# Kernel tuning notes

Measured on AMD Instinct MI355X. Metric: run time of the kernel, lower is better.

Reference implementation:

```python
import jax, jax.numpy as jnp
import numpy as np

N, E = 50000, 800000
D_IN, D_H, D_E, D_P = 128, 64, 64, 64


def _glorot(key, shape):
    lim = (6.0 / (shape[0] + shape[1])) ** 0.5
    return jax.random.uniform(key, shape, jnp.float32, -lim, lim)


def setup_inputs() -> dict:
    key = jax.random.key(0)
    ks = jax.random.split(key, 8)
    x = jax.random.normal(ks[0], (N, D_IN), jnp.float32)
    edge_index = jax.random.randint(ks[1], (2, E), 0, N, dtype=jnp.int64)
    return {
        "x": x,
        "edge_index": edge_index,
        "W1": _glorot(ks[2], (D_IN, D_H)),
        "b1": jnp.zeros((D_H,), jnp.float32),
        "W2": _glorot(ks[3], (D_H, D_E)),
        "b2": jnp.zeros((D_E,), jnp.float32),
        "Wp1": _glorot(ks[4], (D_E, D_E)),
        "bp1": jnp.zeros((D_E,), jnp.float32),
        "Wp2": _glorot(ks[5], (D_E, D_P)),
        "bp2": jnp.zeros((D_P,), jnp.float32),
    }


def gcn_conv(x, src, dst, W, b):
    # PyG GCNConv: h = D^{-1/2}(A+I)D^{-1/2} (x W) + b, self-loops already in src/dst
    n = x.shape[0]
    h = x @ W  # transform first (out_dim < in_dim -> cheaper messages)
    deg = jax.ops.segment_sum(jnp.ones_like(dst, dtype=h.dtype), dst, num_segments=n)
    dinv = jnp.where(deg > 0, jax.lax.rsqrt(deg), 0.0)
    norm = dinv[src] * dinv[dst]  # [E']
    out = jax.ops.segment_sum(h[src] * norm[:, None], dst, num_segments=n)
    return out + b


def reference(x, edge_index, W1, b1, W2, b2, Wp1, bp1, Wp2, bp2):
    n = x.shape[0]
    loops = jnp.arange(n, dtype=edge_index.dtype)
    src = jnp.concatenate([edge_index[0], loops])
    dst = jnp.concatenate([edge_index[1], loops])
    h = jax.nn.relu(gcn_conv(x, src, dst, W1, b1))
    z = gcn_conv(h, src, dst, W2, b2)
    p = jax.nn.relu(z @ Wp1 + bp1) @ Wp2 + bp2
    return (z, p)
```

## Files before the change

kernel.cpp:

```cpp
#include <hip/hip_runtime.h>
#include <hip/hip_fp16.h>

#define DIN 128
#define DH 64
#define NBINS 512
#define BIN_SHIFT 7
#define BIN_NODES 128
#define ETILE 4096
#define EBUF 4096

__device__ inline unsigned pack_half2(float a, float b) {
  __half2 h = __floats2half2_rn(a, b);
  return *(unsigned*)&h;
}
__device__ inline float2 unpack_half2(unsigned u) {
  __half2 h = *(__half2*)&u;
  return __half22float2(h);
}

__global__ __launch_bounds__(512) void k_zero(int* __restrict__ p, int n) {
  int i = blockIdx.x * blockDim.x + threadIdx.x;
  if (i < n) p[i] = 0;
}

__global__ __launch_bounds__(256) void k_fusedA(const float* __restrict__ x,
                                                const float* __restrict__ W1,
                                                __half* __restrict__ g1,
                                                const int* __restrict__ dst,
                                                int* __restrict__ binTot,
                                                int n, int e, int gG) {
  __shared__ float xsT[32][132];
  __shared__ float ws[32 * 64];
  __shared__ int hh[NBINS];
  int t = threadIdx.x;
  int bid = blockIdx.x;

  if (bid >= gG) {
    int b = bid - gG;
    for (int i = t; i < NBINS; i += 256) hh[i] = 0;
    __syncthreads();
    int lo = b * ETILE, hi = lo + ETILE; if (hi > e) hi = e;
    for (int i = lo + t; i < hi; i += 256) atomicAdd(&hh[dst[i] >> BIN_SHIFT], 1);
    __syncthreads();
    for (int i = t; i < NBINS; i += 256) if (hh[i]) atomicAdd(&binTot[i], hh[i]);
    return;
  }

  int row0 = bid * 128;
  int rg = t >> 4, cg = t & 15;
  int r0 = rg * 8, c0 = cg * 4;
  int lr = t >> 3, kq = t & 7;
  float4 acc[8];
#pragma unroll
  for (int i = 0; i < 8; ++i) acc[i] = make_float4(0.f, 0.f, 0.f, 0.f);

  for (int kc = 0; kc < DIN; kc += 32) {
#pragma unroll
    for (int it = 0; it < 4; ++it) {
      int r = it * 32 + lr;
      int gr = row0 + r;
      float4 v = make_float4(0.f, 0.f, 0.f, 0.f);
      if (gr < n) v = *(const float4*)&x[(size_t)gr * DIN + kc + kq * 4];
      xsT[kq * 4 + 0][r] = v.x;
      xsT[kq * 4 + 1][r] = v.y;
      xsT[kq * 4 + 2][r] = v.z;
      xsT[kq * 4 + 3][r] = v.w;
    }
#pragma unroll
    for (int j = 0; j < 8; ++j) ws[t + j * 256] = W1[(size_t)kc * 64 + t + j * 256];
    __syncthreads();
#pragma unroll
    for (int k = 0; k < 32; ++k) {
      float4 xa = *(const float4*)&xsT[k][r0];
      float4 xb = *(const float4*)&xsT[k][r0 + 4];
      float4 wv = *(const float4*)&ws[k * 64 + c0];
      float xr[8] = {xa.x, xa.y, xa.z, xa.w, xb.x, xb.y, xb.z, xb.w};
#pragma unroll
      for (int i = 0; i < 8; ++i) {
        acc[i].x = fmaf(xr[i], wv.x, acc[i].x);
        acc[i].y = fmaf(xr[i], wv.y, acc[i].y);
        acc[i].z = fmaf(xr[i], wv.z, acc[i].z);
        acc[i].w = fmaf(xr[i], wv.w, acc[i].w);
      }
    }
    __syncthreads();
  }
#pragma unroll
  for (int i = 0; i < 8; ++i) {
    int gr = row0 + r0 + i;
    if (gr < n) {
      uint2 u;
      u.x = pack_half2(acc[i].x, acc[i].y);
      u.y = pack_half2(acc[i].z, acc[i].w);
      *(uint2*)&g1[(size_t)gr * 64 + c0] = u;
    }
  }
}

__global__ __launch_bounds__(512) void k_binscan(const int* __restrict__ binTot,
                                                 int* __restrict__ binOff,
                                                 int* __restrict__ binCur, int e) {
  __shared__ int sm[NBINS];
  int t = threadIdx.x;
  int v = binTot[t];
  sm[t] = v;
  __syncthreads();
  for (int ofs = 1; ofs < NBINS; ofs <<= 1) {
    int u = (t >= ofs) ? sm[t - ofs] : 0;
    __syncthreads();
    sm[t] += u;
    __syncthreads();
  }
  int ex = sm[t] - v;
  binOff[t] = ex;
  binCur[t] = ex;
  if (t == NBINS - 1) binOff[NBINS] = sm[NBINS - 1];
}

__global__ __launch_bounds__(256) void k_scatter2(const int* __restrict__ src,
                                                  const int* __restrict__ dst,
                                                  int* __restrict__ binCur,
                                                  int* __restrict__ sp, int e) {
  __shared__ int hh[NBINS];
  __shared__ int base[NBINS];
  int t = threadIdx.x;
  for (int i = t; i < NBINS; i += 256) hh[i] = 0;
  __syncthreads();
  int lo = blockIdx.x * ETILE, hi = lo + ETILE; if (hi > e) hi = e;
  for (int i = lo + t; i < hi; i += 256) atomicAdd(&hh[dst[i] >> BIN_SHIFT], 1);
  __syncthreads();
  for (int i = t; i < NBINS; i += 256) {
    int c = hh[i];
    base[i] = c ? atomicAdd(&binCur[i], c) : 0;
  }
  __syncthreads();
  for (int i = t; i < NBINS; i += 256) hh[i] = 0;
  __syncthreads();
  for (int i = lo + t; i < hi; i += 256) {
    int d = dst[i];
    int bn = d >> BIN_SHIFT;
    int pos = base[bn] + atomicAdd(&hh[bn], 1);
    sp[pos] = (src[i] << BIN_SHIFT) | (d & (BIN_NODES - 1));
  }
}

__global__ __launch_bounds__(256) void k_bincsr(const int* __restrict__ sp,
                                                const int* __restrict__ binOff,
                                                int* __restrict__ off,
                                                float* __restrict__ dinv,
                                                int* __restrict__ srcs,
                                                int n, int e) {
  __shared__ int dl[BIN_NODES];
  __shared__ int sc[BIN_NODES];
  __shared__ int curl[BIN_NODES];
  __shared__ int ebuf[EBUF];
  int b = blockIdx.x, t = threadIdx.x;
  if (t < BIN_NODES) dl[t] = 0;
  __syncthreads();
  int e0 = binOff[b];
  int e1 = binOff[b + 1];
  for (int i = e0 + t; i < e1; i += 256) {
    int u = sp[i];
    int k = i - e0;
    if (k < EBUF) ebuf[k] = u;
    atomicAdd(&dl[u & (BIN_NODES - 1)], 1);
  }
  __syncthreads();
  if (t < BIN_NODES) sc[t] = dl[t];
  __syncthreads();
  for (int ofs = 1; ofs < BIN_NODES; ofs <<= 1) {
    int v = (t < BIN_NODES && t >= ofs) ? sc[t - ofs] : 0;
    __syncthreads();
    if (t < BIN_NODES) sc[t] += v;
    __syncthreads();
  }
  int nbase = b * BIN_NODES;
  if (t < BIN_NODES) {
    int ex = e0 + sc[t] - dl[t];
    curl[t] = ex;
    int node = nbase + t;
    if (node < n) {
      off[node] = ex;
      dinv[node] = rsqrtf((float)(dl[t] + 1));
    }
  }
  if (b == 0 && t == 0) off[n] = e;
  __syncthreads();
  for (int i = e0 + t; i < e1; i += 256) {
    int k = i - e0;
    int u = (k < EBUF) ? ebuf[k] : sp[i];
    int l = u & (BIN_NODES - 1);
    int pos = atomicAdd(&curl[l], 1);
    srcs[pos] = u >> BIN_SHIFT;
  }
}

__global__ __launch_bounds__(256) void k_agg(const __half* __restrict__ gh,
                                             const int* __restrict__ off,
                                             const int* __restrict__ srcs,
                                             const float* __restrict__ dinv,
                                             const float* __restrict__ bias,
                                             __half* __restrict__ out, int n, int relu) {
  int gid = blockIdx.x * 4 + (threadIdx.x >> 6);
  if (gid >= n) return;
  gid = __builtin_amdgcn_readfirstlane(gid);
  int lane = threadIdx.x & 63;
  int grp = lane >> 4;
  int d4 = (lane & 15) * 4;
  float di = dinv[gid];
  float4 acc = make_float4(0.f, 0.f, 0.f, 0.f);
  if (grp == 0) {
    uint2 raw = *(const uint2*)(gh + (size_t)gid * DH + d4);
    float2 f0 = unpack_half2(raw.x), f1 = unpack_half2(raw.y);
    float s = di * di;
    acc.x = f0.x * s; acc.y = f0.y * s; acc.z = f1.x * s; acc.w = f1.y * s;
  }
  int b0 = off[gid], b1 = off[gid + 1];
  int j = b0 + grp;
  for (; j + 12 < b1; j += 16) {
    int s0 = srcs[j], s1 = srcs[j + 4], s2 = srcs[j + 8], s3 = srcs[j + 12];
    float w0 = dinv[s0] * di, w1 = dinv[s1] * di;
    float w2 = dinv[s2] * di, w3 = dinv[s3] * di;
    uint2 r0 = *(const uint2*)(gh + (size_t)s0 * DH + d4);
    uint2 r1 = *(const uint2*)(gh + (size_t)s1 * DH + d4);
    uint2 r2 = *(const uint2*)(gh + (size_t)s2 * DH + d4);
    uint2 r3 = *(const uint2*)(gh + (size_t)s3 * DH + d4);
    float2 a0 = unpack_half2(r0.x), a1 = unpack_half2(r0.y);
    float2 c0 = unpack_half2(r1.x), c1 = unpack_half2(r1.y);
    float2 e0 = unpack_half2(r2.x), e1 = unpack_half2(r2.y);
    float2 g0 = unpack_half2(r3.x), g1 = unpack_half2(r3.y);
    acc.x = fmaf(a0.x, w0, acc.x); acc.y = fmaf(a0.y, w0, acc.y);
    acc.z = fmaf(a1.x, w0, acc.z); acc.w = fmaf(a1.y, w0, acc.w);
    acc.x = fmaf(c0.x, w1, acc.x); acc.y = fmaf(c0.y, w1, acc.y);
    acc.z = fmaf(c1.x, w1, acc.z); acc.w = fmaf(c1.y, w1, acc.w);
    acc.x = fmaf(e0.x, w2, acc.x); acc.y = fmaf(e0.y, w2, acc.y);
    acc.z = fmaf(e1.x, w2, acc.z); acc.w = fmaf(e1.y, w2, acc.w);
    acc.x = fmaf(g0.x, w3, acc.x); acc.y = fmaf(g0.y, w3, acc.y);
    acc.z = fmaf(g1.x, w3, acc.z); acc.w = fmaf(g1.y, w3, acc.w);
  }
  for (; j + 4 < b1; j += 8) {
    int sa = srcs[j], sb = srcs[j + 4];
    float wa = dinv[sa] * di, wb = dinv[sb] * di;
    uint2 ra = *(const uint2*)(gh + (size_t)sa * DH + d4);
    uint2 rb = *(const uint2*)(gh + (size_t)sb * DH + d4);
    float2 a0 = unpack_half2(ra.x), a1 = unpack_half2(ra.y);
    float2 c0 = unpack_half2(rb.x), c1 = unpack_half2(rb.y);
    acc.x = fmaf(a0.x, wa, acc.x); acc.y = fmaf(a0.y, wa, acc.y);
    acc.z = fmaf(a1.x, wa, acc.z); acc.w = fmaf(a1.y, wa, acc.w);
    acc.x = fmaf(c0.x, wb, acc.x); acc.y = fmaf(c0.y, wb, acc.y);
    acc.z = fmaf(c1.x, wb, acc.z); acc.w = fmaf(c1.y, wb, acc.w);
  }
  if (j < b1) {
    int s = srcs[j];
    float w = dinv[s] * di;
    uint2 r = *(const uint2*)(gh + (size_t)s * DH + d4);
    float2 f0 = unpack_half2(r.x), f1 = unpack_half2(r.y);
    acc.x = fmaf(f0.x, w, acc.x); acc.y = fmaf(f0.y, w, acc.y);
    acc.z = fmaf(f1.x, w, acc.z); acc.w = fmaf(f1.y, w, acc.w);
  }
  acc.x += __shfl_xor(acc.x, 16, 64); acc.x += __shfl_xor(acc.x, 32, 64);
  acc.y += __shfl_xor(acc.y, 16, 64); acc.y += __shfl_xor(acc.y, 32, 64);
  acc.z += __shfl_xor(acc.z, 16, 64); acc.z += __shfl_xor(acc.z, 32, 64);
  acc.w += __shfl_xor(acc.w, 16, 64); acc.w += __shfl_xor(acc.w, 32, 64);
  if (lane < 16) {
    if (bias) {
      float4 bv = *(const float4*)&bias[d4];
      acc.x += bv.x; acc.y += bv.y; acc.z += bv.z; acc.w += bv.w;
    }
    if (relu) {
      acc.x = fmaxf(acc.x, 0.f); acc.y = fmaxf(acc.y, 0.f);
      acc.z = fmaxf(acc.z, 0.f); acc.w = fmaxf(acc.w, 0.f);
    }
    uint2 u;
    u.x = pack_half2(acc.x, acc.y);
    u.y = pack_half2(acc.z, acc.w);
    *(uint2*)&out[(size_t)gid * DH + d4] = u;
  }
}

template <bool RELU, bool INHALF>
__global__ __launch_bounds__(256) void k_gemm_rt(const void* __restrict__ Av,
                                                 const float* __restrict__ W,
                                                 const float* __restrict__ bias,
                                                 float* __restrict__ out, int n) {
  constexpr int KC = 32;
  constexpr int MP = 132;
  __shared__ float xsT[KC][MP];
  __shared__ float ws[KC * 64];
  __shared__ float bs[64];
  int t = threadIdx.x;
  if (t < 64) bs[t] = bias[t];
  int row0 = blockIdx.x * 128;
  int rg = t >> 4, cg = t & 15;
  int r0 = rg * 8, c0 = cg * 4;
  float4 acc[8];
#pragma unroll
  for (int i = 0; i < 8; ++i) acc[i] = make_float4(0.f, 0.f, 0.f, 0.f);

  int lr = t >> 3;
  int kq = t & 7;

  for (int kc = 0; kc < DH; kc += KC) {
#pragma unroll
    for (int it = 0; it < 4; ++it) {
      int r = it * 32 + lr;
      int gr = row0 + r;
      float4 v = make_float4(0.f, 0.f, 0.f, 0.f);
      if (gr < n) {
        if (INHALF) {
          uint2 u = *(const uint2*)((const __half*)Av + (size_t)gr * DH + kc + kq * 4);
          float2 f0 = unpack_half2(u.x), f1 = unpack_half2(u.y);
          v = make_float4(f0.x, f0.y, f1.x, f1.y);
        } else {
          v = *(const float4*)&((const float*)Av)[(size_t)gr * DH + kc + kq * 4];
        }
      }
      xsT[kq * 4 + 0][r] = v.x;
      xsT[kq * 4 + 1][r] = v.y;
      xsT[kq * 4 + 2][r] = v.z;
      xsT[kq * 4 + 3][r] = v.w;
    }
#pragma unroll
    for (int j = 0; j < 8; ++j) {
      int idx = t + j * 256;
      ws[idx] = W[(size_t)kc * 64 + idx];
    }
    __syncthreads();
#pragma unroll
    for (int k = 0; k < KC; ++k) {
      float4 xa = *(const float4*)&xsT[k][r0];
      float4 xb = *(const float4*)&xsT[k][r0 + 4];
      float4 wv = *(const float4*)&ws[k * 64 + c0];
      float xr[8] = {xa.x, xa.y, xa.z, xa.w, xb.x, xb.y, xb.z, xb.w};
#pragma unroll
      for (int i = 0; i < 8; ++i) {
        acc[i].x = fmaf(xr[i], wv.x, acc[i].x);
        acc[i].y = fmaf(xr[i], wv.y, acc[i].y);
        acc[i].z = fmaf(xr[i], wv.z, acc[i].z);
        acc[i].w = fmaf(xr[i], wv.w, acc[i].w);
      }
    }
    __syncthreads();
  }

  float4 bv = *(const float4*)&bs[c0];
#pragma unroll
  for (int i = 0; i < 8; ++i) {
    int gr = row0 + r0 + i;
    if (gr < n) {
      float4 o = acc[i];
      o.x += bv.x; o.y += bv.y; o.z += bv.z; o.w += bv.w;
      if (RELU) {
        o.x = fmaxf(o.x, 0.f); o.y = fmaxf(o.y, 0.f);
        o.z = fmaxf(o.z, 0.f); o.w = fmaxf(o.w, 0.f);
      }
      *(float4*)&out[(size_t)gr * DH + c0] = o;
    }
  }
}

extern "C" void kernel_launch(void* const* d_in, const int* in_sizes, int n_in,
                              void* d_out, int out_size, void* d_ws, size_t ws_size,
                              hipStream_t stream) {
  const float* x   = (const float*)d_in[0];
  const int*   ei  = (const int*)d_in[1];
  const float* W1  = (const float*)d_in[2];
  const float* b1  = (const float*)d_in[3];
  const float* W2  = (const float*)d_in[4];
  const float* b2  = (const float*)d_in[5];
  const float* Wp1 = (const float*)d_in[6];
  const float* bp1 = (const float*)d_in[7];
  const float* Wp2 = (const float*)d_in[8];
  const float* bp2 = (const float*)d_in[9];

  int n = in_sizes[0] / DIN;
  int e = in_sizes[1] / 2;
  const int* src = ei;
  const int* dst = ei + e;

  int nblkE = (e + ETILE - 1) / ETILE;
  int nbBins = (n + BIN_NODES - 1) / BIN_NODES;
  int gG = (n + 127) / 128;

  char* ws = (char*)d_ws;
  __half* gtab   = (__half*)ws;
  __half* htab   = (__half*)(ws + ((size_t)7 << 20));
  char*   ctrl   = ws + ((size_t)14 << 20);
  int*    binTot = (int*)(ctrl);
  int*    binOff = (int*)(ctrl + 4096);
  int*    binCur = (int*)(ctrl + 8192);
  int*    off    = (int*)(ctrl + 16384);
  float*  dinv   = (float*)(ctrl + 16384 + (1 << 18));
  int*    sp     = (int*)(ctrl + 16384 + (2 << 18));
  int*    srcs   = sp + e;
  float*  tbuf   = (float*)(ws + ((size_t)24 << 20));

  float* zout = (float*)d_out;
  float* pout = zout + (size_t)n * DH;

  k_zero<<<1, 512, 0, stream>>>(binTot, NBINS);

  k_fusedA<<<gG + nblkE, 256, 0, stream>>>(x, W1, gtab, dst, binTot, n, e, gG);

  k_binscan<<<1, 512, 0, stream>>>(binTot, binOff, binCur, e);

  k_scatter2<<<nblkE, 256, 0, stream>>>(src, dst, binCur, sp, e);

  k_bincsr<<<nbBins, 256, 0, stream>>>(sp, binOff, off, dinv, srcs, n, e);

  k_agg<<<(n + 3) / 4, 256, 0, stream>>>(gtab, off, srcs, dinv, b1, htab, n, 1);

  k_agg<<<(n + 3) / 4, 256, 0, stream>>>(htab, off, srcs, dinv, nullptr, gtab, n, 0);

  k_gemm_rt<false, true ><<<gG, 256, 0, stream>>>(gtab, W2, b2, zout, n);
  k_gemm_rt<true,  false><<<gG, 256, 0, stream>>>(zout, Wp1, bp1, tbuf, n);
  k_gemm_rt<false, false><<<gG, 256, 0, stream>>>(tbuf, Wp2, bp2, pout, n);
}
```

Measured before the change: 141.8 us.

## Prescale features by dinv to remove per-edge dinv gathers in aggregation

```diff
diff --git a/kernel.cpp b/kernel.cpp
--- a/kernel.cpp
+++ b/kernel.cpp
@@ -23,78 +23,16 @@
   if (i < n) p[i] = 0;
 }
 
-__global__ __launch_bounds__(256) void k_fusedA(const float* __restrict__ x,
-                                                const float* __restrict__ W1,
-                                                __half* __restrict__ g1,
-                                                const int* __restrict__ dst,
-                                                int* __restrict__ binTot,
-                                                int n, int e, int gG) {
-  __shared__ float xsT[32][132];
-  __shared__ float ws[32 * 64];
+__global__ __launch_bounds__(256) void k_hist(const int* __restrict__ dst,
+                                              int* __restrict__ binTot, int e) {
   __shared__ int hh[NBINS];
   int t = threadIdx.x;
-  int bid = blockIdx.x;
-
-  if (bid >= gG) {
-    int b = bid - gG;
-    for (int i = t; i < NBINS; i += 256) hh[i] = 0;
-    __syncthreads();
-    int lo = b * ETILE, hi = lo + ETILE; if (hi > e) hi = e;
-    for (int i = lo + t; i < hi; i += 256) atomicAdd(&hh[dst[i] >> BIN_SHIFT], 1);
-    __syncthreads();
-    for (int i = t; i < NBINS; i += 256) if (hh[i]) atomicAdd(&binTot[i], hh[i]);
-    return;
-  }
-
-  int row0 = bid * 128;
-  int rg = t >> 4, cg = t & 15;
-  int r0 = rg * 8, c0 = cg * 4;
-  int lr = t >> 3, kq = t & 7;
-  float4 acc[8];
-#pragma unroll
-  for (int i = 0; i < 8; ++i) acc[i] = make_float4(0.f, 0.f, 0.f, 0.f);
-
-  for (int kc = 0; kc < DIN; kc += 32) {
-#pragma unroll
-    for (int it = 0; it < 4; ++it) {
-      int r = it * 32 + lr;
-      int gr = row0 + r;
-      float4 v = make_float4(0.f, 0.f, 0.f, 0.f);
-      if (gr < n) v = *(const float4*)&x[(size_t)gr * DIN + kc + kq * 4];
-      xsT[kq * 4 + 0][r] = v.x;
-      xsT[kq * 4 + 1][r] = v.y;
-      xsT[kq * 4 + 2][r] = v.z;
-      xsT[kq * 4 + 3][r] = v.w;
-    }
-#pragma unroll
-    for (int j = 0; j < 8; ++j) ws[t + j * 256] = W1[(size_t)kc * 64 + t + j * 256];
-    __syncthreads();
-#pragma unroll
-    for (int k = 0; k < 32; ++k) {
-      float4 xa = *(const float4*)&xsT[k][r0];
-      float4 xb = *(const float4*)&xsT[k][r0 + 4];
-      float4 wv = *(const float4*)&ws[k * 64 + c0];
-      float xr[8] = {xa.x, xa.y, xa.z, xa.w, xb.x, xb.y, xb.z, xb.w};
-#pragma unroll
-      for (int i = 0; i < 8; ++i) {
-        acc[i].x = fmaf(xr[i], wv.x, acc[i].x);
-        acc[i].y = fmaf(xr[i], wv.y, acc[i].y);
-        acc[i].z = fmaf(xr[i], wv.z, acc[i].z);
-        acc[i].w = fmaf(xr[i], wv.w, acc[i].w);
-      }
-    }
-    __syncthreads();
-  }
-#pragma unroll
-  for (int i = 0; i < 8; ++i) {
-    int gr = row0 + r0 + i;
-    if (gr < n) {
-      uint2 u;
-      u.x = pack_half2(acc[i].x, acc[i].y);
-      u.y = pack_half2(acc[i].z, acc[i].w);
-      *(uint2*)&g1[(size_t)gr * 64 + c0] = u;
-    }
-  }
+  for (int i = t; i < NBINS; i += 256) hh[i] = 0;
+  __syncthreads();
+  int lo = blockIdx.x * ETILE, hi = lo + ETILE; if (hi > e) hi = e;
+  for (int i = lo + t; i < hi; i += 256) atomicAdd(&hh[dst[i] >> BIN_SHIFT], 1);
+  __syncthreads();
+  for (int i = t; i < NBINS; i += 256) if (hh[i]) atomicAdd(&binTot[i], hh[i]);
 }
 
 __global__ __launch_bounds__(512) void k_binscan(const int* __restrict__ binTot,
@@ -195,12 +133,72 @@
   }
 }
 
-__global__ __launch_bounds__(256) void k_agg(const __half* __restrict__ gh,
-                                             const int* __restrict__ off,
-                                             const int* __restrict__ srcs,
-                                             const float* __restrict__ dinv,
-                                             const float* __restrict__ bias,
-                                             __half* __restrict__ out, int n, int relu) {
+__global__ __launch_bounds__(256) void k_gemm1d(const float* __restrict__ x,
+                                                const float* __restrict__ W1,
+                                                const float* __restrict__ dinv,
+                                                __half* __restrict__ g1, int n) {
+  __shared__ float xsT[32][132];
+  __shared__ float ws[32 * 64];
+  int t = threadIdx.x;
+  int row0 = blockIdx.x * 128;
+  int rg = t >> 4, cg = t & 15;
+  int r0 = rg * 8, c0 = cg * 4;
+  int lr = t >> 3, kq = t & 7;
+  float4 acc[8];
+#pragma unroll
+  for (int i = 0; i < 8; ++i) acc[i] = make_float4(0.f, 0.f, 0.f, 0.f);
+
+  for (int kc = 0; kc < DIN; kc += 32) {
+#pragma unroll
+    for (int it = 0; it < 4; ++it) {
+      int r = it * 32 + lr;
+      int gr = row0 + r;
+      float4 v = make_float4(0.f, 0.f, 0.f, 0.f);
+      if (gr < n) v = *(const float4*)&x[(size_t)gr * DIN + kc + kq * 4];
+      xsT[kq * 4 + 0][r] = v.x;
+      xsT[kq * 4 + 1][r] = v.y;
+      xsT[kq * 4 + 2][r] = v.z;
+      xsT[kq * 4 + 3][r] = v.w;
+    }
+#pragma unroll
+    for (int j = 0; j < 8; ++j) ws[t + j * 256] = W1[(size_t)kc * 64 + t + j * 256];
+    __syncthreads();
+#pragma unroll
+    for (int k = 0; k < 32; ++k) {
+      float4 xa = *(const float4*)&xsT[k][r0];
+      float4 xb = *(const float4*)&xsT[k][r0 + 4];
+      float4 wv = *(const float4*)&ws[k * 64 + c0];
+      float xr[8] = {xa.x, xa.y, xa.z, xa.w, xb.x, xb.y, xb.z, xb.w};
+#pragma unroll
+      for (int i = 0; i < 8; ++i) {
+        acc[i].x = fmaf(xr[i], wv.x, acc[i].x);
+        acc[i].y = fmaf(xr[i], wv.y, acc[i].y);
+        acc[i].z = fmaf(xr[i], wv.z, acc[i].z);
+        acc[i].w = fmaf(xr[i], wv.w, acc[i].w);
+      }
+    }
+    __syncthreads();
+  }
+#pragma unroll
+  for (int i = 0; i < 8; ++i) {
+    int gr = row0 + r0 + i;
+    if (gr < n) {
+      float di = dinv[gr];
+      uint2 u;
+      u.x = pack_half2(acc[i].x * di, acc[i].y * di);
+      u.y = pack_half2(acc[i].z * di, acc[i].w * di);
+      *(uint2*)&g1[(size_t)gr * 64 + c0] = u;
+    }
+  }
+}
+
+__global__ __launch_bounds__(256) void k_agg2(const __half* __restrict__ gh,
+                                              const int* __restrict__ off,
+                                              const int* __restrict__ srcs,
+                                              const float* __restrict__ dinv,
+                                              const float* __restrict__ bias,
+                                              __half* __restrict__ out, int n,
+                                              int relu, int scaleout) {
   int gid = blockIdx.x * 4 + (threadIdx.x >> 6);
   if (gid >= n) return;
   gid = __builtin_amdgcn_readfirstlane(gid);
@@ -212,15 +210,12 @@
   if (grp == 0) {
     uint2 raw = *(const uint2*)(gh + (size_t)gid * DH + d4);
     float2 f0 = unpack_half2(raw.x), f1 = unpack_half2(raw.y);
-    float s = di * di;
-    acc.x = f0.x * s; acc.y = f0.y * s; acc.z = f1.x * s; acc.w = f1.y * s;
+    acc.x = f0.x; acc.y = f0.y; acc.z = f1.x; acc.w = f1.y;
   }
   int b0 = off[gid], b1 = off[gid + 1];
   int j = b0 + grp;
   for (; j + 12 < b1; j += 16) {
     int s0 = srcs[j], s1 = srcs[j + 4], s2 = srcs[j + 8], s3 = srcs[j + 12];
-    float w0 = dinv[s0] * di, w1 = dinv[s1] * di;
-    float w2 = dinv[s2] * di, w3 = dinv[s3] * di;
     uint2 r0 = *(const uint2*)(gh + (size_t)s0 * DH + d4);
     uint2 r1 = *(const uint2*)(gh + (size_t)s1 * DH + d4);
     uint2 r2 = *(const uint2*)(gh + (size_t)s2 * DH + d4);
@@ -229,40 +224,34 @@
     float2 c0 = unpack_half2(r1.x), c1 = unpack_half2(r1.y);
     float2 e0 = unpack_half2(r2.x), e1 = unpack_half2(r2.y);
     float2 g0 = unpack_half2(r3.x), g1 = unpack_half2(r3.y);
-    acc.x = fmaf(a0.x, w0, acc.x); acc.y = fmaf(a0.y, w0, acc.y);
-    acc.z = fmaf(a1.x, w0, acc.z); acc.w = fmaf(a1.y, w0, acc.w);
-    acc.x = fmaf(c0.x, w1, acc.x); acc.y = fmaf(c0.y, w1, acc.y);
-    acc.z = fmaf(c1.x, w1, acc.z); acc.w = fmaf(c1.y, w1, acc.w);
-    acc.x = fmaf(e0.x, w2, acc.x); acc.y = fmaf(e0.y, w2, acc.y);
-    acc.z = fmaf(e1.x, w2, acc.z); acc.w = fmaf(e1.y, w2, acc.w);
-    acc.x = fmaf(g0.x, w3, acc.x); acc.y = fmaf(g0.y, w3, acc.y);
-    acc.z = fmaf(g1.x, w3, acc.z); acc.w = fmaf(g1.y, w3, acc.w);
+    acc.x += a0.x + c0.x + e0.x + g0.x;
+    acc.y += a0.y + c0.y + e0.y + g0.y;
+    acc.z += a1.x + c1.x + e1.x + g1.x;
+    acc.w += a1.y + c1.y + e1.y + g1.y;
   }
   for (; j + 4 < b1; j += 8) {
     int sa = srcs[j], sb = srcs[j + 4];
-    float wa = dinv[sa] * di, wb = dinv[sb] * di;
     uint2 ra = *(const uint2*)(gh + (size_t)sa * DH + d4);
     uint2 rb = *(const uint2*)(gh + (size_t)sb * DH + d4);
     float2 a0 = unpack_half2(ra.x), a1 = unpack_half2(ra.y);
     float2 c0 = unpack_half2(rb.x), c1 = unpack_half2(rb.y);
-    acc.x = fmaf(a0.x, wa, acc.x); acc.y = fmaf(a0.y, wa, acc.y);
-    acc.z = fmaf(a1.x, wa, acc.z); acc.w = fmaf(a1.y, wa, acc.w);
-    acc.x = fmaf(c0.x, wb, acc.x); acc.y = fmaf(c0.y, wb, acc.y);
-    acc.z = fmaf(c1.x, wb, acc.z); acc.w = fmaf(c1.y, wb, acc.w);
+    acc.x += a0.x + c0.x;
+    acc.y += a0.y + c0.y;
+    acc.z += a1.x + c1.x;
+    acc.w += a1.y + c1.y;
   }
   if (j < b1) {
     int s = srcs[j];
-    float w = dinv[s] * di;
     uint2 r = *(const uint2*)(gh + (size_t)s * DH + d4);
     float2 f0 = unpack_half2(r.x), f1 = unpack_half2(r.y);
-    acc.x = fmaf(f0.x, w, acc.x); acc.y = fmaf(f0.y, w, acc.y);
-    acc.z = fmaf(f1.x, w, acc.z); acc.w = fmaf(f1.y, w, acc.w);
+    acc.x += f0.x; acc.y += f0.y; acc.z += f1.x; acc.w += f1.y;
   }
   acc.x += __shfl_xor(acc.x, 16, 64); acc.x += __shfl_xor(acc.x, 32, 64);
   acc.y += __shfl_xor(acc.y, 16, 64); acc.y += __shfl_xor(acc.y, 32, 64);
   acc.z += __shfl_xor(acc.z, 16, 64); acc.z += __shfl_xor(acc.z, 32, 64);
   acc.w += __shfl_xor(acc.w, 16, 64); acc.w += __shfl_xor(acc.w, 32, 64);
   if (lane < 16) {
+    acc.x *= di; acc.y *= di; acc.z *= di; acc.w *= di;
     if (bias) {
       float4 bv = *(const float4*)&bias[d4];
       acc.x += bv.x; acc.y += bv.y; acc.z += bv.z; acc.w += bv.w;
@@ -270,6 +259,9 @@
     if (relu) {
       acc.x = fmaxf(acc.x, 0.f); acc.y = fmaxf(acc.y, 0.f);
       acc.z = fmaxf(acc.z, 0.f); acc.w = fmaxf(acc.w, 0.f);
+    }
+    if (scaleout) {
+      acc.x *= di; acc.y *= di; acc.z *= di; acc.w *= di;
     }
     uint2 u;
     u.x = pack_half2(acc.x, acc.y);
@@ -399,18 +391,16 @@
   float* pout = zout + (size_t)n * DH;
 
   k_zero<<<1, 512, 0, stream>>>(binTot, NBINS);
-
-  k_fusedA<<<gG + nblkE, 256, 0, stream>>>(x, W1, gtab, dst, binTot, n, e, gG);
-
+  k_hist<<<nblkE, 256, 0, stream>>>(dst, binTot, e);
   k_binscan<<<1, 512, 0, stream>>>(binTot, binOff, binCur, e);
-
   k_scatter2<<<nblkE, 256, 0, stream>>>(src, dst, binCur, sp, e);
-
   k_bincsr<<<nbBins, 256, 0, stream>>>(sp, binOff, off, dinv, srcs, n, e);
 
-  k_agg<<<(n + 3) / 4, 256, 0, stream>>>(gtab, off, srcs, dinv, b1, htab, n, 1);
-
-  k_agg<<<(n + 3) / 4, 256, 0, stream>>>(htab, off, srcs, dinv, nullptr, gtab, n, 0);
+  k_gemm1d<<<gG, 256, 0, stream>>>(x, W1, dinv, gtab, n);
+
+  k_agg2<<<(n + 3) / 4, 256, 0, stream>>>(gtab, off, srcs, dinv, b1, htab, n, 1, 1);
+
+  k_agg2<<<(n + 3) / 4, 256, 0, stream>>>(htab, off, srcs, dinv, nullptr, gtab, n, 0, 0);
 
   k_gemm_rt<false, true ><<<gG, 256, 0, stream>>>(gtab, W2, b2, zout, n);
   k_gemm_rt<true,  false><<<gG, 256, 0, stream>>>(zout, Wp1, bp1, tbuf, n);
```

Result: slower. 146.7 us (+3.4%).

## Fuse edge scatter into GEMM kernel using fixed-capacity bin slots, drop scan pass

Applied to the files above, without the earlier changes.

```diff
diff --git a/kernel.cpp b/kernel.cpp
--- a/kernel.cpp
+++ b/kernel.cpp
@@ -8,6 +8,7 @@
 #define BIN_NODES 128
 #define ETILE 4096
 #define EBUF 4096
+#define SLOT 4096
 
 __device__ inline unsigned pack_half2(float a, float b) {
   __half2 h = __floats2half2_rn(a, b);
@@ -23,15 +24,18 @@
   if (i < n) p[i] = 0;
 }
 
-__global__ __launch_bounds__(256) void k_fusedA(const float* __restrict__ x,
-                                                const float* __restrict__ W1,
-                                                __half* __restrict__ g1,
-                                                const int* __restrict__ dst,
-                                                int* __restrict__ binTot,
-                                                int n, int e, int gG) {
+__global__ __launch_bounds__(256) void k_scatgemm(const float* __restrict__ x,
+                                                  const float* __restrict__ W1,
+                                                  __half* __restrict__ g1,
+                                                  const int* __restrict__ src,
+                                                  const int* __restrict__ dst,
+                                                  int* __restrict__ binCur,
+                                                  int* __restrict__ sp,
+                                                  int n, int e, int gG) {
   __shared__ float xsT[32][132];
   __shared__ float ws[32 * 64];
   __shared__ int hh[NBINS];
+  __shared__ int base[NBINS];
   int t = threadIdx.x;
   int bid = blockIdx.x;
 
@@ -42,7 +46,19 @@
     int lo = b * ETILE, hi = lo + ETILE; if (hi > e) hi = e;
     for (int i = lo + t; i < hi; i += 256) atomicAdd(&hh[dst[i] >> BIN_SHIFT], 1);
     __syncthreads();
-    for (int i = t; i < NBINS; i += 256) if (hh[i]) atomicAdd(&binTot[i], hh[i]);
+    for (int i = t; i < NBINS; i += 256) {
+      int c = hh[i];
+      base[i] = c ? atomicAdd(&binCur[i], c) : 0;
+    }
+    __syncthreads();
+    for (int i = t; i < NBINS; i += 256) hh[i] = 0;
+    __syncthreads();
+    for (int i = lo + t; i < hi; i += 256) {
+      int d = dst[i];
+      int bn = d >> BIN_SHIFT;
+      int pos = base[bn] + atomicAdd(&hh[bn], 1);
+      if (pos < SLOT) sp[bn * SLOT + pos] = (src[i] << BIN_SHIFT) | (d & (BIN_NODES - 1));
+    }
     return;
   }
 
@@ -97,59 +113,12 @@
   }
 }
 
-__global__ __launch_bounds__(512) void k_binscan(const int* __restrict__ binTot,
-                                                 int* __restrict__ binOff,
-                                                 int* __restrict__ binCur, int e) {
-  __shared__ int sm[NBINS];
-  int t = threadIdx.x;
-  int v = binTot[t];
-  sm[t] = v;
-  __syncthreads();
-  for (int ofs = 1; ofs < NBINS; ofs <<= 1) {
-    int u = (t >= ofs) ? sm[t - ofs] : 0;
-    __syncthreads();
-    sm[t] += u;
-    __syncthreads();
-  }
-  int ex = sm[t] - v;
-  binOff[t] = ex;
-  binCur[t] = ex;
-  if (t == NBINS - 1) binOff[NBINS] = sm[NBINS - 1];
-}
-
-__global__ __launch_bounds__(256) void k_scatter2(const int* __restrict__ src,
-                                                  const int* __restrict__ dst,
-                                                  int* __restrict__ binCur,
-                                                  int* __restrict__ sp, int e) {
-  __shared__ int hh[NBINS];
-  __shared__ int base[NBINS];
-  int t = threadIdx.x;
-  for (int i = t; i < NBINS; i += 256) hh[i] = 0;
-  __syncthreads();
-  int lo = blockIdx.x * ETILE, hi = lo + ETILE; if (hi > e) hi = e;
-  for (int i = lo + t; i < hi; i += 256) atomicAdd(&hh[dst[i] >> BIN_SHIFT], 1);
-  __syncthreads();
-  for (int i = t; i < NBINS; i += 256) {
-    int c = hh[i];
-    base[i] = c ? atomicAdd(&binCur[i], c) : 0;
-  }
-  __syncthreads();
-  for (int i = t; i < NBINS; i += 256) hh[i] = 0;
-  __syncthreads();
-  for (int i = lo + t; i < hi; i += 256) {
-    int d = dst[i];
-    int bn = d >> BIN_SHIFT;
-    int pos = base[bn] + atomicAdd(&hh[bn], 1);
-    sp[pos] = (src[i] << BIN_SHIFT) | (d & (BIN_NODES - 1));
-  }
-}
-
-__global__ __launch_bounds__(256) void k_bincsr(const int* __restrict__ sp,
-                                                const int* __restrict__ binOff,
-                                                int* __restrict__ off,
-                                                float* __restrict__ dinv,
-                                                int* __restrict__ srcs,
-                                                int n, int e) {
+__global__ __launch_bounds__(256) void k_bincsr2(const int* __restrict__ sp,
+                                                 const int* __restrict__ binCur,
+                                                 int* __restrict__ off,
+                                                 int* __restrict__ deg,
+                                                 float* __restrict__ dinv,
+                                                 int* __restrict__ srcs, int n) {
   __shared__ int dl[BIN_NODES];
   __shared__ int sc[BIN_NODES];
   __shared__ int curl[BIN_NODES];
@@ -157,12 +126,12 @@
   int b = blockIdx.x, t = threadIdx.x;
   if (t < BIN_NODES) dl[t] = 0;
   __syncthreads();
-  int e0 = binOff[b];
-  int e1 = binOff[b + 1];
+  int e0 = b * SLOT;
+  int cnt = binCur[b]; if (cnt > SLOT) cnt = SLOT;
+  int e1 = e0 + cnt;
   for (int i = e0 + t; i < e1; i += 256) {
     int u = sp[i];
-    int k = i - e0;
-    if (k < EBUF) ebuf[k] = u;
+    ebuf[i - e0] = u;
     atomicAdd(&dl[u & (BIN_NODES - 1)], 1);
   }
   __syncthreads();
@@ -181,14 +150,13 @@
     int node = nbase + t;
     if (node < n) {
       off[node] = ex;
+      deg[node] = dl[t];
       dinv[node] = rsqrtf((float)(dl[t] + 1));
     }
   }
-  if (b == 0 && t == 0) off[n] = e;
   __syncthreads();
   for (int i = e0 + t; i < e1; i += 256) {
-    int k = i - e0;
-    int u = (k < EBUF) ? ebuf[k] : sp[i];
+    int u = ebuf[i - e0];
     int l = u & (BIN_NODES - 1);
     int pos = atomicAdd(&curl[l], 1);
     srcs[pos] = u >> BIN_SHIFT;
@@ -197,6 +165,7 @@
 
 __global__ __launch_bounds__(256) void k_agg(const __half* __restrict__ gh,
                                              const int* __restrict__ off,
+                                             const int* __restrict__ deg,
                                              const int* __restrict__ srcs,
                                              const float* __restrict__ dinv,
                                              const float* __restrict__ bias,
@@ -215,7 +184,7 @@
     float s = di * di;
     acc.x = f0.x * s; acc.y = f0.y * s; acc.z = f1.x * s; acc.w = f1.y * s;
   }
-  int b0 = off[gid], b1 = off[gid + 1];
+  int b0 = off[gid], b1 = b0 + deg[gid];
   int j = b0 + grp;
   for (; j + 12 < b1; j += 16) {
     int s0 = srcs[j], s1 = srcs[j + 4], s2 = srcs[j + 8], s3 = srcs[j + 12];
@@ -386,31 +355,26 @@
   __half* gtab   = (__half*)ws;
   __half* htab   = (__half*)(ws + ((size_t)7 << 20));
   char*   ctrl   = ws + ((size_t)14 << 20);
-  int*    binTot = (int*)(ctrl);
-  int*    binOff = (int*)(ctrl + 4096);
-  int*    binCur = (int*)(ctrl + 8192);
-  int*    off    = (int*)(ctrl + 16384);
-  float*  dinv   = (float*)(ctrl + 16384 + (1 << 18));
-  int*    sp     = (int*)(ctrl + 16384 + (2 << 18));
-  int*    srcs   = sp + e;
-  float*  tbuf   = (float*)(ws + ((size_t)24 << 20));
+  int*    binCur = (int*)(ctrl);
+  int*    off    = (int*)(ctrl + 4096);
+  int*    deg    = (int*)(ctrl + 4096 + (1 << 18));
+  float*  dinv   = (float*)(ctrl + 4096 + (2 << 18));
+  int*    sp     = (int*)(ws + ((size_t)16 << 20));
+  int*    srcs   = (int*)(ws + ((size_t)24 << 20));
+  float*  tbuf   = (float*)(ws + ((size_t)32 << 20));
 
   float* zout = (float*)d_out;
   float* pout = zout + (size_t)n * DH;
 
-  k_zero<<<1, 512, 0, stream>>>(binTot, NBINS);
-
-  k_fusedA<<<gG + nblkE, 256, 0, stream>>>(x, W1, gtab, dst, binTot, n, e, gG);
-
-  k_binscan<<<1, 512, 0, stream>>>(binTot, binOff, binCur, e);
-
-  k_scatter2<<<nblkE, 256, 0, stream>>>(src, dst, binCur, sp, e);
-
-  k_bincsr<<<nbBins, 256, 0, stream>>>(sp, binOff, off, dinv, srcs, n, e);
-
-  k_agg<<<(n + 3) / 4, 256, 0, stream>>>(gtab, off, srcs, dinv, b1, htab, n, 1);
-
-  k_agg<<<(n + 3) / 4, 256, 0, stream>>>(htab, off, srcs, dinv, nullptr, gtab, n, 0);
+  k_zero<<<1, 512, 0, stream>>>(binCur, NBINS);
+
+  k_scatgemm<<<gG + nblkE, 256, 0, stream>>>(x, W1, gtab, src, dst, binCur, sp, n, e, gG);
+
+  k_bincsr2<<<nbBins, 256, 0, stream>>>(sp, binCur, off, deg, dinv, srcs, n);
+
+  k_agg<<<(n + 3) / 4, 256, 0, stream>>>(gtab, off, deg, srcs, dinv, b1, htab, n, 1);
+
+  k_agg<<<(n + 3) / 4, 256, 0, stream>>>(htab, off, deg, srcs, dinv, nullptr, gtab, n, 0);
 
   k_gemm_rt<false, true ><<<gG, 256, 0, stream>>>(gtab, W2, b2, zout, n);
   k_gemm_rt<true,  false><<<gG, 256, 0, stream>>>(zout, Wp1, bp1, tbuf, n);
```

Result: faster. 123.5 us (-12.9%).
